# Performance work log

Measured on AMD Instinct MI355X. Metric: run time of the kernel, lower is better.

## Reference

```python
import jax, jax.numpy as jnp
import numpy as np

LMAX = 2
MUL = 8          # output_size: multiplicity of edge irreps on both TP inputs
COUT = 16        # channels_out
NB = 16          # number_of_basis
MAX_R = 5.0
NUM_PATHS = 15   # all (l1,l2,l3) triangle-valid paths with l<=2
# lexicographic path order: (0,0,0),(0,1,1),(0,2,2),(1,0,1),(1,1,0),(1,1,1),(1,1,2),
# (1,2,1),(1,2,2),(2,0,2),(2,1,1),(2,1,2),(2,2,0),(2,2,1),(2,2,2)
# x2 is zero for l2>0 (only x2[0]=Ai[dst]), so only (l,0,l) paths contribute:
PATH_IDX = {0: 0, 1: 3, 2: 9}
PATH_NORM = 1.0 / np.sqrt(MUL * MUL)  # per-path weight normalization


def silu(x):
    return jax.nn.silu(x)


def sph_harmonics(n):
    """Real spherical harmonics (component-normalized) of unit vectors n (E,3), l=0..2."""
    x, y, z = n[:, 0], n[:, 1], n[:, 2]
    Y0 = jnp.ones_like(x)[:, None]
    Y1 = jnp.sqrt(3.0) * n
    Y2 = jnp.stack([
        jnp.sqrt(15.0) * x * y,
        jnp.sqrt(15.0) * y * z,
        (jnp.sqrt(5.0) / 2.0) * (3.0 * z * z - 1.0),  # |n|=1
        jnp.sqrt(15.0) * x * z,
        (jnp.sqrt(15.0) / 2.0) * (x * x - y * y),
    ], axis=-1)
    return [Y0, Y1, Y2]


def soft_one_hot_gaussian(x, start, end, number):
    # e3nn soft_one_hot_linspace, basis='gaussian', cutoff=True
    values = jnp.linspace(start, end, number + 2)[1:-1]
    step = values[1] - values[0]
    diff = (x[:, None] - values) / step
    return jnp.exp(-diff * diff) / 1.12


def setup_inputs() -> dict:
    key = jax.random.key(0)
    ks = jax.random.split(key, 24)
    N, E, G = 50000, 800000, 64
    inp = {}
    inp["pos"] = jax.random.normal(ks[0], (N, 3), jnp.float32) * 3.0
    inp["A"] = jax.random.randint(ks[1], (N,), 0, 10)
    inp["batch"] = jnp.sort(jax.random.randint(ks[2], (N,), 0, G))
    inp["edge_src"] = jax.random.randint(ks[3], (E,), 0, N)
    inp["edge_dst"] = jax.random.randint(ks[4], (E,), 0, N)
    inp["edge_shifts"] = jnp.zeros((E, 3), jnp.float32)
    inp["cell"] = jax.random.normal(ks[5], (G, 3, 3), jnp.float32)
    # learned parameters
    inp["emb_table"] = jax.random.normal(ks[6], (10, 16), jnp.float32)
    inp["atom_w1"] = jax.random.normal(ks[7], (16, 64), jnp.float32) / 4.0
    inp["atom_b1"] = jnp.zeros((64,), jnp.float32)
    inp["atom_w2"] = jax.random.normal(ks[8], (64, MUL), jnp.float32) / 8.0
    inp["atom_b2"] = jnp.zeros((MUL,), jnp.float32)
    inp["fc_w1"] = jax.random.normal(ks[9], (NB, 64), jnp.float32) / 4.0
    inp["fc_b1"] = jnp.zeros((64,), jnp.float32)
    inp["fc_w2"] = jax.random.normal(ks[10], (64, 64), jnp.float32) / 8.0
    inp["fc_b2"] = jnp.zeros((64,), jnp.float32)
    inp["fc_w3"] = jax.random.normal(ks[11], (64, NUM_PATHS), jnp.float32) / 8.0
    inp["fc_b3"] = jnp.zeros((NUM_PATHS,), jnp.float32)
    inp["tp_w"] = jax.random.normal(ks[12], (NUM_PATHS, MUL, MUL, COUT), jnp.float32)
    return inp


def reference(pos, A, batch, edge_src, edge_dst, edge_shifts, cell,
              emb_table, atom_w1, atom_b1, atom_w2, atom_b2,
              fc_w1, fc_b1, fc_w2, fc_b2, fc_w3, fc_b3, tp_w):
    N = pos.shape[0]
    # --- edge geometry (PBC) ---
    edge_cells = cell[batch[edge_src]]                      # (E,3,3)
    shift_vecs = jnp.einsum('ei,eij->ej', edge_shifts, edge_cells)
    edge_vec = pos[edge_dst] - pos[edge_src] + shift_vecs    # (E,3)
    edge_length = jnp.sqrt(jnp.sum(edge_vec * edge_vec, axis=-1))
    n = edge_vec / jnp.maximum(edge_length, 1e-8)[:, None]
    # --- node scalars ---
    h = silu(emb_table[A] @ atom_w1 + atom_b1)
    Ai = h @ atom_w2 + atom_b2                               # (N,MUL)
    # --- spherical harmonics / per-edge irreps ---
    Y = sph_harmonics(n)                                     # list of (E,2l+1)
    Ai_src = Ai[edge_src]                                    # (E,MUL)
    x2_0 = Ai[edge_dst]                                      # (E,MUL) = only nonzero block of input 2
    # --- radial gates ---
    emb = soft_one_hot_gaussian(edge_length, 0.0, MAX_R, NB) * np.sqrt(NB)
    g = silu(emb @ fc_w1 + fc_b1)
    g = silu(g @ fc_w2 + fc_b2)
    gates = g @ fc_w3 + fc_b3                                # (E,NUM_PATHS)
    # --- tensor product: f_in[l] (x) x2[0] -> out[l]; only (l,0,l) paths survive ---
    out_parts = []
    for l in range(LMAX + 1):
        f_l = Ai_src[:, :, None] * Y[l][:, None, :]          # (E,MUL,2l+1)
        W = tp_w[PATH_IDX[l]]                                 # (MUL,MUL,COUT)
        mixed = jnp.einsum('ev,uvw->euw', x2_0, W)            # (E,MUL,COUT)
        o = jnp.einsum('eui,euw->ewi', f_l, mixed)            # (E,COUT,2l+1)
        o = o * (gates[:, PATH_IDX[l]][:, None, None] * PATH_NORM)
        out_parts.append(o.reshape(o.shape[0], COUT * (2 * l + 1)))
    edge_features = jnp.concatenate(out_parts, axis=-1)      # (E, COUT*9)
    # --- mean aggregation onto destination nodes ---
    ones = jnp.ones((edge_dst.shape[0],), edge_features.dtype)
    count = jnp.clip(jax.ops.segment_sum(ones, edge_dst, num_segments=N), 1.0)
    out = jax.ops.segment_sum(edge_features, edge_dst, num_segments=N) / count[:, None]
    return out
```

## Files before the change

### kernel.cpp

```cpp
#include <hip/hip_runtime.h>
#include <hip/hip_bf16.h>
#include <math.h>

#define MUL 8
#define NCOL 144
#define TSIZE 8192
#define TMAXLEN 8.0f
#define STG 68

__device__ __forceinline__ float silu_f(float x) { return x / (1.0f + __expf(-x)); }

__global__ void node_mlp_kernel(const int* __restrict__ A,
                                const float* __restrict__ emb_table,
                                const float* __restrict__ w1,
                                const float* __restrict__ b1,
                                const float* __restrict__ w2,
                                const float* __restrict__ b2,
                                float* __restrict__ Ai, int N) {
    __shared__ float s_w1[16 * 64];
    __shared__ float s_w2[64 * MUL];
    __shared__ float s_b1[64];
    __shared__ float s_b2[MUL];
    __shared__ float s_emb[10 * 16];
    for (int i = threadIdx.x; i < 16 * 64; i += blockDim.x) s_w1[i] = w1[i];
    for (int i = threadIdx.x; i < 64 * MUL; i += blockDim.x) s_w2[i] = w2[i];
    for (int i = threadIdx.x; i < 64; i += blockDim.x) s_b1[i] = b1[i];
    for (int i = threadIdx.x; i < MUL; i += blockDim.x) s_b2[i] = b2[i];
    for (int i = threadIdx.x; i < 160; i += blockDim.x) s_emb[i] = emb_table[i];
    __syncthreads();

    int n = blockIdx.x * blockDim.x + threadIdx.x;
    if (n >= N) return;
    int a = A[n];

    float h[64];
    #pragma unroll
    for (int j = 0; j < 64; j++) h[j] = s_b1[j];
    #pragma unroll 1
    for (int k = 0; k < 16; k++) {
        float ek = s_emb[a * 16 + k];
        #pragma unroll
        for (int j = 0; j < 64; j++) h[j] += ek * s_w1[k * 64 + j];
    }
    #pragma unroll
    for (int j = 0; j < 64; j++) h[j] = silu_f(h[j]);

    #pragma unroll 1
    for (int u = 0; u < MUL; u++) {
        float acc = s_b2[u];
        #pragma unroll
        for (int k = 0; k < 64; k++) acc += h[k] * s_w2[k * MUL + u];
        Ai[n * MUL + u] = acc;
    }
}

__global__ void __launch_bounds__(256) prologue2_kernel(
        const int* __restrict__ edst, const float* __restrict__ shifts,
        const float* __restrict__ emb_table,
        const float* __restrict__ aw1, const float* __restrict__ ab1,
        const float* __restrict__ aw2, const float* __restrict__ ab2,
        const float* __restrict__ fw1, const float* __restrict__ fb1,
        const float* __restrict__ fw2, const float* __restrict__ fb2,
        const float* __restrict__ fw3, const float* __restrict__ fb3,
        const float* __restrict__ tpw,
        int* __restrict__ count, int* __restrict__ rank, int* __restrict__ flag,
        float* __restrict__ At, float4* __restrict__ tab,
        float* __restrict__ tpwT, int E) {
    int b = blockIdx.x;
    if (b < 32) {
        int i = b * 256 + threadIdx.x;
        if (i >= TSIZE) return;
        float len = (float)i * (TMAXLEN / TSIZE);
        float r = len * (17.0f / 5.0f);
        float h[64];
        #pragma unroll
        for (int j = 0; j < 64; j++) h[j] = fb1[j];
        #pragma unroll 1
        for (int k = 0; k < 16; k++) {
            float dk = r - (float)(k + 1);
            float ek = __expf(-dk * dk) * (4.0f / 1.12f);
            #pragma unroll
            for (int j = 0; j < 64; j++) h[j] += ek * fw1[k * 64 + j];
        }
        #pragma unroll
        for (int j = 0; j < 64; j++) h[j] = silu_f(h[j]);
        float g0 = fb3[0], g1 = fb3[3], g2 = fb3[9];
        #pragma unroll 1
        for (int j = 0; j < 64; j++) {
            float a = fb2[j];
            #pragma unroll
            for (int k = 0; k < 64; k++) a += h[k] * fw2[k * 64 + j];
            a = silu_f(a);
            g0 += a * fw3[j * 15 + 0];
            g1 += a * fw3[j * 15 + 3];
            g2 += a * fw3[j * 15 + 9];
        }
        tab[i] = make_float4(g0 * 0.125f, g1 * 0.125f, g2 * 0.125f, 0.f);
    } else if (b == 32) {
        const int pl[3] = {0, 3, 9};
        for (int i = threadIdx.x; i < 3072; i += 256) {
            int l = i >> 10, r = i & 1023;
            int u = r >> 7, v = (r >> 4) & 7, w = r & 15;
            tpwT[(l << 10) + (u << 7) + (w << 3) + v] = tpw[pl[l] * 1024 + r];
        }
        int t = threadIdx.x;
        if (t < 80) {
            int ty = t >> 3, u = t & 7;
            float h[64];
            #pragma unroll
            for (int j = 0; j < 64; j++) h[j] = ab1[j];
            #pragma unroll 1
            for (int k = 0; k < 16; k++) {
                float ek = emb_table[ty * 16 + k];
                #pragma unroll
                for (int j = 0; j < 64; j++) h[j] += ek * aw1[k * 64 + j];
            }
            #pragma unroll
            for (int j = 0; j < 64; j++) h[j] = silu_f(h[j]);
            float acc = ab2[u];
            #pragma unroll
            for (int k = 0; k < 64; k++) acc += h[k] * aw2[k * MUL + u];
            At[ty * 8 + u] = acc;
        }
    } else {
        int e = (b - 33) * 256 + threadIdx.x;
        bool nz = false;
        if (e < E) {
            int d = edst[e];
            float sh0 = shifts[e * 3 + 0], sh1 = shifts[e * 3 + 1], sh2 = shifts[e * 3 + 2];
            nz = (sh0 != 0.f) || (sh1 != 0.f) || (sh2 != 0.f);
            rank[e] = atomicAdd(&count[d], 1);
        }
        if (__ballot(nz)) {
            if ((threadIdx.x & 63) == 0) atomicOr(flag, 1);
        }
    }
}

__global__ void count_kernel(const int* __restrict__ edst, int* __restrict__ count, int E) {
    int e = blockIdx.x * blockDim.x + threadIdx.x;
    if (e < E) atomicAdd(&count[edst[e]], 1);
}

__global__ void scan_kernel(const int* __restrict__ count, int* __restrict__ off, int N) {
    __shared__ int sums[1024];
    int L = N + 1;
    int chunk = (L + 1023) / 1024;
    int t = threadIdx.x;
    int lo = t * chunk;
    int hi = lo + chunk; if (hi > L) hi = L;
    int local = 0;
    for (int i = lo; i < hi; i++) local += (i < N) ? count[i] : 0;
    sums[t] = local;
    __syncthreads();
    for (int s = 1; s < 1024; s <<= 1) {
        int v = (t >= s) ? sums[t - s] : 0;
        __syncthreads();
        sums[t] += v;
        __syncthreads();
    }
    int run = (t == 0) ? 0 : sums[t - 1];
    for (int i = lo; i < hi; i++) {
        off[i] = run;
        run += (i < N) ? count[i] : 0;
    }
}

__global__ void __launch_bounds__(256) scan_part_kernel(
        const int* __restrict__ count, int* __restrict__ bsum, int N) {
    __shared__ int red[256];
    int t = threadIdx.x;
    int idx = blockIdx.x * 256 + t;
    red[t] = (idx < N) ? count[idx] : 0;
    __syncthreads();
    #pragma unroll
    for (int s = 128; s > 0; s >>= 1) {
        if (t < s) red[t] += red[t + s];
        __syncthreads();
    }
    if (t == 0) bsum[blockIdx.x] = red[0];
}

__global__ void __launch_bounds__(1024) scan_top_kernel(
        const int* __restrict__ bsum, int* __restrict__ bpre,
        int* __restrict__ off, int N, int nblk) {
    __shared__ int s[1024];
    int t = threadIdx.x;
    int v = (t < nblk) ? bsum[t] : 0;
    s[t] = v;
    __syncthreads();
    for (int d = 1; d < 1024; d <<= 1) {
        int x = (t >= d) ? s[t - d] : 0;
        __syncthreads();
        s[t] += x;
        __syncthreads();
    }
    if (t < nblk) bpre[t] = s[t] - v;
    if (t == 1023) off[N] = s[1023];
}

__global__ void __launch_bounds__(256) scan_write_kernel(
        const int* __restrict__ count, const int* __restrict__ bpre,
        int* __restrict__ off, int N) {
    __shared__ int s[256];
    int t = threadIdx.x;
    int idx = blockIdx.x * 256 + t;
    int c = (idx < N) ? count[idx] : 0;
    s[t] = c;
    __syncthreads();
    for (int d = 1; d < 256; d <<= 1) {
        int x = (t >= d) ? s[t - d] : 0;
        __syncthreads();
        s[t] += x;
        __syncthreads();
    }
    if (idx < N) off[idx] = bpre[blockIdx.x] + s[t] - c;
}

__global__ void fill_kernel(const int* __restrict__ edst, const int* __restrict__ off,
                            int* __restrict__ cursor, int* __restrict__ list, int E) {
    int e = blockIdx.x * blockDim.x + threadIdx.x;
    if (e >= E) return;
    int d = edst[e];
    int p = atomicAdd(&cursor[d], 1);
    list[off[d] + p] = e;
}

__global__ void __launch_bounds__(256) permute_kernel(
        const int* __restrict__ edst, const int* __restrict__ esrc,
        const int* __restrict__ rank, const int* __restrict__ off,
        const int* __restrict__ flagp, int* __restrict__ list, int E) {
    int e = blockIdx.x * 256 + threadIdx.x;
    if (e >= E) return;
    int d = edst[e];
    int p = off[d] + rank[e];
    list[p] = (*flagp) ? e : esrc[e];
}

__global__ void __launch_bounds__(256) conv_at_kernel(
        const float* __restrict__ pos, const int* __restrict__ batch,
        const int* __restrict__ esrc,
        const float* __restrict__ shifts, const float* __restrict__ cell,
        const int* __restrict__ A, const float* __restrict__ At,
        const float* __restrict__ tpwT, const float4* __restrict__ gtab,
        const int* __restrict__ flagp, const int* __restrict__ off,
        const int* __restrict__ list,
        float* __restrict__ out, int N) {
    __shared__ float s_stage[4][17 * STG];
    __shared__ float s_Z[4][288];
    __shared__ float s_M[4][388];
    __shared__ float s_Ad[4][32];

    const int tid = threadIdx.x, wv = tid >> 6, lane = tid & 63;
    const int k = lane >> 4, s = lane & 15;
    const int base = blockIdx.x * 16 + wv * 4;
    const int n = base + k;
    const bool nv = (n < N);

    const int FL = *flagp;

    int b0 = nv ? off[n] : 0;
    int b1 = nv ? off[n + 1] : 0;
    int deg = b1 - b0;

    if (s < 8) {
        int an = nv ? A[n] : 0;
        s_Ad[wv][k * 8 + s] = nv ? At[an * 8 + s] : 0.f;
    }

    float px = 0.f, py = 0.f, pz = 0.f;
    if (nv && deg > 0) { px = pos[n * 3 + 0]; py = pos[n * 3 + 1]; pz = pos[n * 3 + 2]; }

    int md = deg;
    md = max(md, __shfl_xor(md, 16));
    md = max(md, __shfl_xor(md, 32));
    int nrnd = (md + 15) >> 4;

    float* st = s_stage[wv];

    float z[5];
    const float4* ruP[5];
    const float4* riP[5];
    #pragma unroll
    for (int j = 0; j < 5; j++) {
        int p = s + 16 * j;
        int u = (p < 72) ? (p / 9) : 0;
        int i = (p < 72) ? (p - 9 * u) : 0;
        ruP[j] = (const float4*)(st + u * STG + k * 16);
        riP[j] = (const float4*)(st + (8 + i) * STG + k * 16);
        z[j] = 0.f;
    }

    #pragma unroll 1
    for (int rnd = 0; rnd < nrnd; rnd++) {
        int sl = (rnd << 4) + s;
        float As[8], gy[9];
        #pragma unroll
        for (int u = 0; u < 8; u++) As[u] = 0.f;
        #pragma unroll
        for (int i = 0; i < 9; i++) gy[i] = 0.f;
        if (sl < deg) {
            int v = list[b0 + sl];
            int src;
            float sv0 = 0.f, sv1 = 0.f, sv2 = 0.f;
            if (FL) {
                int e = v;
                src = esrc[e];
                float sh0 = shifts[e * 3 + 0], sh1 = shifts[e * 3 + 1], sh2 = shifts[e * 3 + 2];
                if (sh0 != 0.f || sh1 != 0.f || sh2 != 0.f) {
                    int g = batch[src];
                    const float* cg = cell + g * 9;
                    sv0 = sh0 * cg[0] + sh1 * cg[3] + sh2 * cg[6];
                    sv1 = sh0 * cg[1] + sh1 * cg[4] + sh2 * cg[7];
                    sv2 = sh0 * cg[2] + sh1 * cg[5] + sh2 * cg[8];
                }
            } else {
                src = v;
            }
            float vx = px - pos[src * 3 + 0] + sv0;
            float vy = py - pos[src * 3 + 1] + sv1;
            float vz = pz - pos[src * 3 + 2] + sv2;
            float len = sqrtf(vx * vx + vy * vy + vz * vz);
            float inv = 1.0f / fmaxf(len, 1e-8f);
            float nx = vx * inv, ny = vy * inv, nz = vz * inv;

            float tp = fminf(len * ((float)TSIZE / TMAXLEN), (float)(TSIZE - 1));
            int ti = (int)tp; if (ti > TSIZE - 2) ti = TSIZE - 2;
            float fr = tp - (float)ti;
            float4 ga = gtab[ti], gb = gtab[ti + 1];
            float g0 = ga.x + fr * (gb.x - ga.x);
            float g1 = ga.y + fr * (gb.y - ga.y);
            float g2 = ga.z + fr * (gb.z - ga.z);

            const float s3c = 1.7320508075688772f;
            const float s15 = 3.872983346207417f;
            const float s5h = 1.118033988749895f;
            gy[0] = g0;
            gy[1] = g1 * (s3c * nx); gy[2] = g1 * (s3c * ny); gy[3] = g1 * (s3c * nz);
            gy[4] = g2 * (s15 * nx * ny); gy[5] = g2 * (s15 * ny * nz);
            gy[6] = g2 * (s5h * (3.f * nz * nz - 1.f));
            gy[7] = g2 * (s15 * nx * nz); gy[8] = g2 * (0.5f * s15 * (nx * nx - ny * ny));

            int a = A[src];
            const float4* Ap = (const float4*)(At + a * 8);
            float4 A0 = Ap[0], A1 = Ap[1];
            As[0] = A0.x; As[1] = A0.y; As[2] = A0.z; As[3] = A0.w;
            As[4] = A1.x; As[5] = A1.y; As[6] = A1.z; As[7] = A1.w;
        }
        #pragma unroll
        for (int u = 0; u < 8; u++) st[u * STG + lane] = As[u];
        #pragma unroll
        for (int i = 0; i < 9; i++) st[(8 + i) * STG + lane] = gy[i];
        __builtin_amdgcn_wave_barrier();
        #pragma unroll
        for (int j = 0; j < 5; j++) {
            if (j < 4 || s < 8) {
                #pragma unroll
                for (int c = 0; c < 4; c++) {
                    float4 a = ruP[j][c], b = riP[j][c];
                    z[j] += a.x * b.x + a.y * b.y + a.z * b.z + a.w * b.w;
                }
            }
        }
        __builtin_amdgcn_wave_barrier();
    }

    #pragma unroll
    for (int j = 0; j < 5; j++)
        if (j < 4 || s < 8) s_Z[wv][k * 72 + s + 16 * j] = z[j];
    __builtin_amdgcn_wave_barrier();

    const float4* twp[6];
    int moff[6];
    #pragma unroll
    for (int t = 0; t < 6; t++) {
        int m = lane + (t << 6);
        int l = m >> 7, r = m & 127, u = r >> 4, w = r & 15;
        twp[t] = (const float4*)(tpwT + (l << 10) + (u << 7) + (w << 3));
        moff[t] = (l << 7) + (w << 3) + u;
    }
    int moffo[3], zoff[3];
    bool ov[3];
    #pragma unroll
    for (int t = 0; t < 3; t++) {
        int c = lane + (t << 6);
        ov[t] = (c < NCOL);
        int cc = ov[t] ? c : 0;
        int l, w, ii;
        if (cc < 16)      { l = 0; w = cc;            ii = 0; }
        else if (cc < 64) { l = 1; w = (cc - 16) / 3; ii = 1 + (cc - 16) % 3; }
        else              { l = 2; w = (cc - 64) / 5; ii = 4 + (cc - 64) % 5; }
        moffo[t] = (l << 7) + (w << 3);
        zoff[t] = ii;
    }

    float* M = s_M[wv];
    float* Zb = s_Z[wv];
    #pragma unroll 1
    for (int k2 = 0; k2 < 4; k2++) {
        int nk = base + k2;
        float Adk[8];
        #pragma unroll
        for (int v = 0; v < 8; v++) Adk[v] = s_Ad[wv][k2 * 8 + v];
        #pragma unroll
        for (int t = 0; t < 6; t++) {
            float4 wa = twp[t][0], wb = twp[t][1];
            M[moff[t]] = Adk[0] * wa.x + Adk[1] * wa.y + Adk[2] * wa.z + Adk[3] * wa.w
                       + Adk[4] * wb.x + Adk[5] * wb.y + Adk[6] * wb.z + Adk[7] * wb.w;
        }
        int degk = __shfl(deg, k2 * 16);
        __builtin_amdgcn_wave_barrier();
        if (nk < N) {
            float dinv = 1.0f / fmaxf((float)degk, 1.0f);
            const float* Zk = Zb + k2 * 72;
            #pragma unroll
            for (int t = 0; t < 3; t++) {
                if (ov[t]) {
                    const float4* mm = (const float4*)(M + moffo[t]);
                    float4 m0 = mm[0], m1 = mm[1];
                    int ii = zoff[t];
                    float val = m0.x * Zk[0 + ii]  + m0.y * Zk[9 + ii]
                              + m0.z * Zk[18 + ii] + m0.w * Zk[27 + ii]
                              + m1.x * Zk[36 + ii] + m1.y * Zk[45 + ii]
                              + m1.z * Zk[54 + ii] + m1.w * Zk[63 + ii];
                    out[(size_t)nk * NCOL + lane + (t << 6)] = val * dinv;
                }
            }
        }
        __builtin_amdgcn_wave_barrier();
    }
}

__global__ void __launch_bounds__(256) prologue_kernel(
        const int* __restrict__ A, const float* __restrict__ emb_table,
        const float* __restrict__ aw1, const float* __restrict__ ab1,
        const float* __restrict__ aw2, const float* __restrict__ ab2,
        const float* __restrict__ fw1, const float* __restrict__ fb1,
        const float* __restrict__ fw2, const float* __restrict__ fb2,
        const float* __restrict__ fw3, const float* __restrict__ fb3,
        const float* __restrict__ tpw,
        float* __restrict__ Ai, float4* __restrict__ tab,
        float* __restrict__ tpwT, int N) {
    __shared__ float s_w1[16 * 64];
    __shared__ float s_w2[64 * MUL];
    __shared__ float s_b1[64];
    __shared__ float s_b2[MUL];
    __shared__ float s_emb[10 * 16];

    int b = blockIdx.x;
    if (b < 32) {
        int i = b * 256 + threadIdx.x;
        if (i >= TSIZE) return;
        float len = (float)i * (TMAXLEN / TSIZE);
        float r = len * (17.0f / 5.0f);
        float h[64];
        #pragma unroll
        for (int j = 0; j < 64; j++) h[j] = fb1[j];
        #pragma unroll 1
        for (int k = 0; k < 16; k++) {
            float dk = r - (float)(k + 1);
            float ek = __expf(-dk * dk) * (4.0f / 1.12f);
            #pragma unroll
            for (int j = 0; j < 64; j++) h[j] += ek * fw1[k * 64 + j];
        }
        #pragma unroll
        for (int j = 0; j < 64; j++) h[j] = silu_f(h[j]);
        float g0 = fb3[0], g1 = fb3[3], g2 = fb3[9];
        #pragma unroll 1
        for (int j = 0; j < 64; j++) {
            float a = fb2[j];
            #pragma unroll
            for (int k = 0; k < 64; k++) a += h[k] * fw2[k * 64 + j];
            a = silu_f(a);
            g0 += a * fw3[j * 15 + 0];
            g1 += a * fw3[j * 15 + 3];
            g2 += a * fw3[j * 15 + 9];
        }
        tab[i] = make_float4(g0 * 0.125f, g1 * 0.125f, g2 * 0.125f, 0.f);
    } else if (b == 32) {
        const int pl[3] = {0, 3, 9};
        for (int i = threadIdx.x; i < 3072; i += 256) {
            int l = i >> 10, r = i & 1023;
            int u = r >> 7, v = (r >> 4) & 7, w = r & 15;
            tpwT[(l << 10) + (u << 7) + (w << 3) + v] = tpw[pl[l] * 1024 + r];
        }
    } else {
        for (int i = threadIdx.x; i < 16 * 64; i += 256) s_w1[i] = aw1[i];
        for (int i = threadIdx.x; i < 64 * MUL; i += 256) s_w2[i] = aw2[i];
        for (int i = threadIdx.x; i < 64; i += 256) s_b1[i] = ab1[i];
        for (int i = threadIdx.x; i < MUL; i += 256) s_b2[i] = ab2[i];
        for (int i = threadIdx.x; i < 160; i += 256) s_emb[i] = emb_table[i];
        __syncthreads();

        int n = (b - 33) * 256 + threadIdx.x;
        if (n >= N) return;
        int a = A[n];

        float h[64];
        #pragma unroll
        for (int j = 0; j < 64; j++) h[j] = s_b1[j];
        #pragma unroll 1
        for (int k = 0; k < 16; k++) {
            float ek = s_emb[a * 16 + k];
            #pragma unroll
            for (int j = 0; j < 64; j++) h[j] += ek * s_w1[k * 64 + j];
        }
        #pragma unroll
        for (int j = 0; j < 64; j++) h[j] = silu_f(h[j]);

        #pragma unroll 1
        for (int u = 0; u < MUL; u++) {
            float acc = s_b2[u];
            #pragma unroll
            for (int k = 0; k < 64; k++) acc += h[k] * s_w2[k * MUL + u];
            Ai[n * MUL + u] = acc;
        }
    }
}

__global__ void __launch_bounds__(256) conv_node4_kernel(
        const float* __restrict__ pos, const int* __restrict__ batch,
        const int* __restrict__ esrc,
        const float* __restrict__ shifts, const float* __restrict__ cell,
        const float* __restrict__ tpwT, const float4* __restrict__ gtab,
        const float* __restrict__ Ai, const int* __restrict__ off,
        const int* __restrict__ list,
        float* __restrict__ out, int N) {
    __shared__ float s_stage[4][17 * STG];
    __shared__ float s_Z[4][288];
    __shared__ float s_M[4][388];
    __shared__ float s_Ad[4][32];

    const int tid = threadIdx.x, wv = tid >> 6, lane = tid & 63;
    const int k = lane >> 4, s = lane & 15;
    const int base = blockIdx.x * 16 + wv * 4;
    const int n = base + k;
    const bool nv = (n < N);

    int b0 = nv ? off[n] : 0;
    int b1 = nv ? off[n + 1] : 0;
    int deg = b1 - b0;

    if (s < 8) s_Ad[wv][k * 8 + s] = nv ? Ai[(size_t)n * MUL + s] : 0.f;

    float px = 0.f, py = 0.f, pz = 0.f;
    if (nv && deg > 0) { px = pos[n * 3 + 0]; py = pos[n * 3 + 1]; pz = pos[n * 3 + 2]; }

    int md = deg;
    md = max(md, __shfl_xor(md, 16));
    md = max(md, __shfl_xor(md, 32));
    int nrnd = (md + 15) >> 4;

    float* st = s_stage[wv];

    float z[5];
    const float4* ruP[5];
    const float4* riP[5];
    #pragma unroll
    for (int j = 0; j < 5; j++) {
        int p = s + 16 * j;
        int u = (p < 72) ? (p / 9) : 0;
        int i = (p < 72) ? (p - 9 * u) : 0;
        ruP[j] = (const float4*)(st + u * STG + k * 16);
        riP[j] = (const float4*)(st + (8 + i) * STG + k * 16);
        z[j] = 0.f;
    }

    #pragma unroll 1
    for (int rnd = 0; rnd < nrnd; rnd++) {
        int sl = (rnd << 4) + s;
        float As[8], gy[9];
        #pragma unroll
        for (int u = 0; u < 8; u++) As[u] = 0.f;
        #pragma unroll
        for (int i = 0; i < 9; i++) gy[i] = 0.f;
        if (sl < deg) {
            int e = list[b0 + sl];
            float sh0 = shifts[e * 3 + 0], sh1 = shifts[e * 3 + 1], sh2 = shifts[e * 3 + 2];
            int src = esrc[e];
            float sv0 = 0.f, sv1 = 0.f, sv2 = 0.f;
            if (sh0 != 0.f || sh1 != 0.f || sh2 != 0.f) {
                int g = batch[src];
                const float* cg = cell + g * 9;
                sv0 = sh0 * cg[0] + sh1 * cg[3] + sh2 * cg[6];
                sv1 = sh0 * cg[1] + sh1 * cg[4] + sh2 * cg[7];
                sv2 = sh0 * cg[2] + sh1 * cg[5] + sh2 * cg[8];
            }
            float vx = px - pos[src * 3 + 0] + sv0;
            float vy = py - pos[src * 3 + 1] + sv1;
            float vz = pz - pos[src * 3 + 2] + sv2;
            float len = sqrtf(vx * vx + vy * vy + vz * vz);
            float inv = 1.0f / fmaxf(len, 1e-8f);
            float nx = vx * inv, ny = vy * inv, nz = vz * inv;

            float tp = fminf(len * ((float)TSIZE / TMAXLEN), (float)(TSIZE - 1));
            int ti = (int)tp; if (ti > TSIZE - 2) ti = TSIZE - 2;
            float fr = tp - (float)ti;
            float4 ga = gtab[ti], gb = gtab[ti + 1];
            float g0 = ga.x + fr * (gb.x - ga.x);
            float g1 = ga.y + fr * (gb.y - ga.y);
            float g2 = ga.z + fr * (gb.z - ga.z);

            const float s3c = 1.7320508075688772f;
            const float s15 = 3.872983346207417f;
            const float s5h = 1.118033988749895f;
            gy[0] = g0;
            gy[1] = g1 * (s3c * nx); gy[2] = g1 * (s3c * ny); gy[3] = g1 * (s3c * nz);
            gy[4] = g2 * (s15 * nx * ny); gy[5] = g2 * (s15 * ny * nz);
            gy[6] = g2 * (s5h * (3.f * nz * nz - 1.f));
            gy[7] = g2 * (s15 * nx * nz); gy[8] = g2 * (0.5f * s15 * (nx * nx - ny * ny));

            const float4* Ap = (const float4*)(Ai + (size_t)src * MUL);
            float4 A0 = Ap[0], A1 = Ap[1];
            As[0] = A0.x; As[1] = A0.y; As[2] = A0.z; As[3] = A0.w;
            As[4] = A1.x; As[5] = A1.y; As[6] = A1.z; As[7] = A1.w;
        }
        #pragma unroll
        for (int u = 0; u < 8; u++) st[u * STG + lane] = As[u];
        #pragma unroll
        for (int i = 0; i < 9; i++) st[(8 + i) * STG + lane] = gy[i];
        __builtin_amdgcn_wave_barrier();
        #pragma unroll
        for (int j = 0; j < 5; j++) {
            if (j < 4 || s < 8) {
                #pragma unroll
                for (int c = 0; c < 4; c++) {
                    float4 a = ruP[j][c], b = riP[j][c];
                    z[j] += a.x * b.x + a.y * b.y + a.z * b.z + a.w * b.w;
                }
            }
        }
        __builtin_amdgcn_wave_barrier();
    }

    #pragma unroll
    for (int j = 0; j < 5; j++)
        if (j < 4 || s < 8) s_Z[wv][k * 72 + s + 16 * j] = z[j];
    __builtin_amdgcn_wave_barrier();

    const float4* twp[6];
    int moff[6];
    #pragma unroll
    for (int t = 0; t < 6; t++) {
        int m = lane + (t << 6);
        int l = m >> 7, r = m & 127, u = r >> 4, w = r & 15;
        twp[t] = (const float4*)(tpwT + (l << 10) + (u << 7) + (w << 3));
        moff[t] = (l << 7) + (w << 3) + u;
    }
    int moffo[3], zoff[3];
    bool ov[3];
    #pragma unroll
    for (int t = 0; t < 3; t++) {
        int c = lane + (t << 6);
        ov[t] = (c < NCOL);
        int cc = ov[t] ? c : 0;
        int l, w, ii;
        if (cc < 16)      { l = 0; w = cc;            ii = 0; }
        else if (cc < 64) { l = 1; w = (cc - 16) / 3; ii = 1 + (cc - 16) % 3; }
        else              { l = 2; w = (cc - 64) / 5; ii = 4 + (cc - 64) % 5; }
        moffo[t] = (l << 7) + (w << 3);
        zoff[t] = ii;
    }

    float* M = s_M[wv];
    float* Zb = s_Z[wv];
    #pragma unroll 1
    for (int k2 = 0; k2 < 4; k2++) {
        int nk = base + k2;
        float Adk[8];
        #pragma unroll
        for (int v = 0; v < 8; v++) Adk[v] = s_Ad[wv][k2 * 8 + v];
        #pragma unroll
        for (int t = 0; t < 6; t++) {
            float4 wa = twp[t][0], wb = twp[t][1];
            M[moff[t]] = Adk[0] * wa.x + Adk[1] * wa.y + Adk[2] * wa.z + Adk[3] * wa.w
                       + Adk[4] * wb.x + Adk[5] * wb.y + Adk[6] * wb.z + Adk[7] * wb.w;
        }
        int degk = __shfl(deg, k2 * 16);
        __builtin_amdgcn_wave_barrier();
        if (nk < N) {
            float dinv = 1.0f / fmaxf((float)degk, 1.0f);
            const float* Zk = Zb + k2 * 72;
            #pragma unroll
            for (int t = 0; t < 3; t++) {
                if (ov[t]) {
                    const float4* mm = (const float4*)(M + moffo[t]);
                    float4 m0 = mm[0], m1 = mm[1];
                    int ii = zoff[t];
                    float val = m0.x * Zk[0 + ii]  + m0.y * Zk[9 + ii]
                              + m0.z * Zk[18 + ii] + m0.w * Zk[27 + ii]
                              + m1.x * Zk[36 + ii] + m1.y * Zk[45 + ii]
                              + m1.z * Zk[54 + ii] + m1.w * Zk[63 + ii];
                    out[(size_t)nk * NCOL + lane + (t << 6)] = val * dinv;
                }
            }
        }
        __builtin_amdgcn_wave_barrier();
    }
}

__global__ void __launch_bounds__(256) edge_atomic_kernel(
        const float* __restrict__ pos, const int* __restrict__ batch,
        const int* __restrict__ esrc, const int* __restrict__ edst,
        const float* __restrict__ shifts, const float* __restrict__ cell,
        const float* __restrict__ fw1, const float* __restrict__ fb1,
        const float* __restrict__ fw2, const float* __restrict__ fb2,
        const float* __restrict__ fw3, const float* __restrict__ fb3,
        const float* __restrict__ tpw,
        const float* __restrict__ Ai,
        float* __restrict__ out, float* __restrict__ deg, int E) {
    __shared__ float s_w1[16 * 64];
    __shared__ float s_w2[64 * 64];
    __shared__ float s_w3[64 * 3];
    __shared__ float s_b1[64];
    __shared__ float s_b2[64];
    __shared__ float s_b3[3];
    __shared__ float s_tpw[3 * 1024];
    for (int i = threadIdx.x; i < 1024; i += blockDim.x) s_w1[i] = fw1[i];
    for (int i = threadIdx.x; i < 4096; i += blockDim.x) s_w2[i] = fw2[i];
    for (int i = threadIdx.x; i < 64; i += blockDim.x) { s_b1[i] = fb1[i]; s_b2[i] = fb2[i]; }
    for (int i = threadIdx.x; i < 192; i += blockDim.x) {
        int j = i / 3, c = i - 3 * j;
        int cc = (c == 0) ? 0 : ((c == 1) ? 3 : 9);
        s_w3[i] = fw3[j * 15 + cc];
    }
    if (threadIdx.x < 3) {
        int cc = (threadIdx.x == 0) ? 0 : ((threadIdx.x == 1) ? 3 : 9);
        s_b3[threadIdx.x] = fb3[cc];
    }
    for (int i = threadIdx.x; i < 3 * 1024; i += blockDim.x) {
        int l = i >> 10, r = i & 1023;
        int p = (l == 0) ? 0 : ((l == 1) ? 3 : 9);
        s_tpw[i] = tpw[p * 1024 + r];
    }
    __syncthreads();
    int e = blockIdx.x * blockDim.x + threadIdx.x;
    if (e >= E) return;
    int s = esrc[e], d = edst[e];
    int g = batch[s];
    float sh0 = shifts[e * 3 + 0], sh1 = shifts[e * 3 + 1], sh2 = shifts[e * 3 + 2];
    const float* cg = cell + g * 9;
    float sv0 = sh0 * cg[0] + sh1 * cg[3] + sh2 * cg[6];
    float sv1 = sh0 * cg[1] + sh1 * cg[4] + sh2 * cg[7];
    float sv2 = sh0 * cg[2] + sh1 * cg[5] + sh2 * cg[8];
    float vx = pos[d * 3 + 0] - pos[s * 3 + 0] + sv0;
    float vy = pos[d * 3 + 1] - pos[s * 3 + 1] + sv1;
    float vz = pos[d * 3 + 2] - pos[s * 3 + 2] + sv2;
    float len = sqrtf(vx * vx + vy * vy + vz * vz);
    float inv = 1.0f / fmaxf(len, 1e-8f);
    float nx = vx * inv, ny = vy * inv, nz = vz * inv;
    float r = len * (17.0f / 5.0f);
    float h[64];
    #pragma unroll
    for (int j = 0; j < 64; j++) h[j] = s_b1[j];
    #pragma unroll 1
    for (int k = 0; k < 16; k++) {
        float dk = r - (float)(k + 1);
        float ek = __expf(-dk * dk) * (4.0f / 1.12f);
        #pragma unroll
        for (int j = 0; j < 64; j++) h[j] += ek * s_w1[k * 64 + j];
    }
    #pragma unroll
    for (int j = 0; j < 64; j++) h[j] = silu_f(h[j]);
    float g0 = s_b3[0], g1 = s_b3[1], g2 = s_b3[2];
    #pragma unroll 2
    for (int j = 0; j < 64; j++) {
        float a = s_b2[j];
        #pragma unroll
        for (int k = 0; k < 64; k++) a += h[k] * s_w2[k * 64 + j];
        a = silu_f(a);
        g0 += a * s_w3[j * 3 + 0];
        g1 += a * s_w3[j * 3 + 1];
        g2 += a * s_w3[j * 3 + 2];
    }
    g0 *= 0.125f; g1 *= 0.125f; g2 *= 0.125f;
    float t0[16], t1[16], t2[16];
    #pragma unroll
    for (int w = 0; w < 16; w++) { t0[w] = 0.f; t1[w] = 0.f; t2[w] = 0.f; }
    int s8 = s * MUL, d8 = d * MUL;
    float Ad[8];
    #pragma unroll
    for (int v = 0; v < 8; v++) Ad[v] = Ai[d8 + v];
    #pragma unroll 1
    for (int u = 0; u < 8; u++) {
        float asu = Ai[s8 + u];
        int offp = u * 128;
        #pragma unroll
        for (int v = 0; v < 8; v++) {
            float p = asu * Ad[v];
            int o2 = offp + v * 16;
            #pragma unroll
            for (int w = 0; w < 16; w++) {
                t0[w] += p * s_tpw[o2 + w];
                t1[w] += p * s_tpw[1024 + o2 + w];
                t2[w] += p * s_tpw[2048 + o2 + w];
            }
        }
    }
    #pragma unroll
    for (int w = 0; w < 16; w++) { t0[w] *= g0; t1[w] *= g1; t2[w] *= g2; }
    const float s3 = 1.7320508075688772f;
    const float s15 = 3.872983346207417f;
    const float s5h = 1.118033988749895f;
    float y1_[3] = { s3 * nx, s3 * ny, s3 * nz };
    float y2_[5] = { s15 * nx * ny, s15 * ny * nz, s5h * (3.f * nz * nz - 1.f),
                     s15 * nx * nz, 0.5f * s15 * (nx * nx - ny * ny) };
    float* o = out + (size_t)d * NCOL;
    #pragma unroll
    for (int w = 0; w < 16; w++) atomicAdd(o + w, t0[w]);
    #pragma unroll
    for (int w = 0; w < 16; w++)
        #pragma unroll
        for (int i = 0; i < 3; i++) atomicAdd(o + 16 + w * 3 + i, t1[w] * y1_[i]);
    #pragma unroll
    for (int w = 0; w < 16; w++)
        #pragma unroll
        for (int i = 0; i < 5; i++) atomicAdd(o + 64 + w * 5 + i, t2[w] * y2_[i]);
    atomicAdd(deg + d, 1.0f);
}

__global__ void finalize_kernel(float* __restrict__ out, const float* __restrict__ deg, int total) {
    int idx = blockIdx.x * blockDim.x + threadIdx.x;
    if (idx >= total) return;
    int n = idx / NCOL;
    out[idx] = out[idx] / fmaxf(deg[n], 1.0f);
}

extern "C" void kernel_launch(void* const* d_in, const int* in_sizes, int n_in,
                              void* d_out, int out_size, void* d_ws, size_t ws_size,
                              hipStream_t stream) {
    const float* pos    = (const float*)d_in[0];
    const int*   A      = (const int*)d_in[1];
    const int*   batch  = (const int*)d_in[2];
    const int*   esrc   = (const int*)d_in[3];
    const int*   edst   = (const int*)d_in[4];
    const float* shifts = (const float*)d_in[5];
    const float* cellp  = (const float*)d_in[6];
    const float* embt   = (const float*)d_in[7];
    const float* aw1    = (const float*)d_in[8];
    const float* ab1    = (const float*)d_in[9];
    const float* aw2    = (const float*)d_in[10];
    const float* ab2    = (const float*)d_in[11];
    const float* fw1    = (const float*)d_in[12];
    const float* fb1    = (const float*)d_in[13];
    const float* fw2    = (const float*)d_in[14];
    const float* fb2    = (const float*)d_in[15];
    const float* fw3    = (const float*)d_in[16];
    const float* fb3    = (const float*)d_in[17];
    const float* tpw    = (const float*)d_in[18];

    int N = in_sizes[1];
    int E = in_sizes[3];
    float* out = (float*)d_out;

    int nblk = (N + 255) / 256;
    int eblk = (E + 255) / 256;

    size_t need_new = ((size_t)N + 1 + (size_t)(N + 1) + (size_t)E * 2) * 4
                    + (size_t)TSIZE * 16 + 3072 * 4 + 320 + 8192 + 768;
    size_t need_mid = (size_t)N * 32 + (size_t)N * 8 + (size_t)(N + 1) * 4
                    + (size_t)E * 4 + (size_t)TSIZE * 16 + 3072 * 4 + 8192 + 1024;

    if (ws_size >= need_new && nblk <= 1024) {
        int*    count = (int*)d_ws;
        int*    flag  = count + N;
        int*    off   = flag + 1;
        int*    rank  = off + (N + 1);
        int*    list  = rank + E;
        float4* gtab  = (float4*)(((uintptr_t)(list + E) + 255) & ~(uintptr_t)255);
        float*  tpwT  = (float*)(gtab + TSIZE);
        float*  At    = tpwT + 3072;
        int*    bsum  = (int*)(At + 80);
        int*    bpre  = bsum + 1024;

        hipMemsetAsync(count, 0, ((size_t)N + 1) * sizeof(int), stream);

        prologue2_kernel<<<33 + eblk, 256, 0, stream>>>(
            edst, shifts, embt, aw1, ab1, aw2, ab2,
            fw1, fb1, fw2, fb2, fw3, fb3, tpw,
            count, rank, flag, At, gtab, tpwT, E);

        scan_part_kernel<<<nblk, 256, 0, stream>>>(count, bsum, N);
        scan_top_kernel<<<1, 1024, 0, stream>>>(bsum, bpre, off, N, nblk);
        scan_write_kernel<<<nblk, 256, 0, stream>>>(count, bpre, off, N);

        permute_kernel<<<eblk, 256, 0, stream>>>(edst, esrc, rank, off, flag, list, E);

        conv_at_kernel<<<(N + 15) / 16, 256, 0, stream>>>(
            pos, batch, esrc, shifts, cellp, A, At, tpwT, gtab, flag, off, list, out, N);
    } else if (ws_size >= need_mid) {
        float*  Ai     = (float*)d_ws;
        int*    count  = (int*)(Ai + (size_t)N * MUL);
        int*    cursor = count + N;
        int*    off    = cursor + N;
        int*    list   = off + (N + 1);
        float4* gtab   = (float4*)(((uintptr_t)(list + E) + 255) & ~(uintptr_t)255);
        float*  tpwT   = (float*)(gtab + TSIZE);
        int*    bsum   = (int*)(tpwT + 3072);
        int*    bpre   = bsum + 1024;

        hipMemsetAsync(count, 0, (size_t)N * 2 * sizeof(int), stream);

        prologue_kernel<<<33 + nblk, 256, 0, stream>>>(
            A, embt, aw1, ab1, aw2, ab2, fw1, fb1, fw2, fb2, fw3, fb3,
            tpw, Ai, gtab, tpwT, N);
        count_kernel<<<eblk, 256, 0, stream>>>(edst, count, E);

        if (nblk <= 1024) {
            scan_part_kernel<<<nblk, 256, 0, stream>>>(count, bsum, N);
            scan_top_kernel<<<1, 1024, 0, stream>>>(bsum, bpre, off, N, nblk);
            scan_write_kernel<<<nblk, 256, 0, stream>>>(count, bpre, off, N);
        } else {
            scan_kernel<<<1, 1024, 0, stream>>>(count, off, N);
        }

        fill_kernel<<<eblk, 256, 0, stream>>>(edst, off, cursor, list, E);

        conv_node4_kernel<<<(N + 15) / 16, 256, 0, stream>>>(
            pos, batch, esrc, shifts, cellp, tpwT, gtab, Ai, off, list, out, N);
    } else {
        float* Ai  = (float*)d_ws;
        float* deg = Ai + (size_t)N * MUL;
        hipMemsetAsync(out, 0, (size_t)out_size * sizeof(float), stream);
        hipMemsetAsync(deg, 0, (size_t)N * sizeof(float), stream);
        node_mlp_kernel<<<(N + 255) / 256, 256, 0, stream>>>(A, embt, aw1, ab1, aw2, ab2, Ai, N);
        edge_atomic_kernel<<<eblk, 256, 0, stream>>>(
            pos, batch, esrc, edst, shifts, cellp,
            fw1, fb1, fw2, fb2, fw3, fb3, tpw, Ai, out, deg, E);
        int total = N * NCOL;
        finalize_kernel<<<(total + 255) / 256, 256, 0, stream>>>(out, deg, total);
    }
}
```

Measured before the change: 218.1 us.

## Parallelize gate-table MLP across wavefront lanes instead of per-thread serial loops

```diff
diff --git a/kernel.cpp b/kernel.cpp
--- a/kernel.cpp
+++ b/kernel.cpp
@@ -7,6 +7,7 @@
 #define TSIZE 8192
 #define TMAXLEN 8.0f
 #define STG 68
+#define GBLK 512
 
 __device__ __forceinline__ float silu_f(float x) { return x / (1.0f + __expf(-x)); }
 
@@ -54,7 +55,7 @@
     }
 }
 
-__global__ void __launch_bounds__(256) prologue2_kernel(
+__global__ void __launch_bounds__(256) front_kernel(
         const int* __restrict__ edst, const float* __restrict__ shifts,
         const float* __restrict__ emb_table,
         const float* __restrict__ aw1, const float* __restrict__ ab1,
@@ -66,64 +67,68 @@
         int* __restrict__ count, int* __restrict__ rank, int* __restrict__ flag,
         float* __restrict__ At, float4* __restrict__ tab,
         float* __restrict__ tpwT, int E) {
-    int b = blockIdx.x;
-    if (b < 32) {
-        int i = b * 256 + threadIdx.x;
-        if (i >= TSIZE) return;
-        float len = (float)i * (TMAXLEN / TSIZE);
-        float r = len * (17.0f / 5.0f);
-        float h[64];
-        #pragma unroll
-        for (int j = 0; j < 64; j++) h[j] = fb1[j];
+    const int b = blockIdx.x;
+    const int lane = threadIdx.x & 63, wv = threadIdx.x >> 6;
+
+    if (b < GBLK) {
+        int gw = b * 4 + wv;
         #pragma unroll 1
-        for (int k = 0; k < 16; k++) {
-            float dk = r - (float)(k + 1);
-            float ek = __expf(-dk * dk) * (4.0f / 1.12f);
-            #pragma unroll
-            for (int j = 0; j < 64; j++) h[j] += ek * fw1[k * 64 + j];
-        }
-        #pragma unroll
-        for (int j = 0; j < 64; j++) h[j] = silu_f(h[j]);
-        float g0 = fb3[0], g1 = fb3[3], g2 = fb3[9];
-        #pragma unroll 1
-        for (int j = 0; j < 64; j++) {
-            float a = fb2[j];
-            #pragma unroll
-            for (int k = 0; k < 64; k++) a += h[k] * fw2[k * 64 + j];
+        for (int e = gw; e < TSIZE; e += GBLK * 4) {
+            float len = (float)e * (TMAXLEN / TSIZE);
+            float r = len * (17.0f / 5.0f);
+            float h = fb1[lane];
+            #pragma unroll
+            for (int k = 0; k < 16; k++) {
+                float dk = r - (float)(k + 1);
+                float ek = __expf(-dk * dk) * (4.0f / 1.12f);
+                h += ek * fw1[k * 64 + lane];
+            }
+            h = silu_f(h);
+            float a = fb2[lane];
+            #pragma unroll
+            for (int k = 0; k < 64; k++) a += __shfl(h, k) * fw2[k * 64 + lane];
             a = silu_f(a);
-            g0 += a * fw3[j * 15 + 0];
-            g1 += a * fw3[j * 15 + 3];
-            g2 += a * fw3[j * 15 + 9];
-        }
-        tab[i] = make_float4(g0 * 0.125f, g1 * 0.125f, g2 * 0.125f, 0.f);
-    } else if (b == 32) {
+            float g0 = a * fw3[lane * 15 + 0];
+            float g1 = a * fw3[lane * 15 + 3];
+            float g2 = a * fw3[lane * 15 + 9];
+            #pragma unroll
+            for (int off = 32; off > 0; off >>= 1) {
+                g0 += __shfl_xor(g0, off);
+                g1 += __shfl_xor(g1, off);
+                g2 += __shfl_xor(g2, off);
+            }
+            if (lane == 0)
+                tab[e] = make_float4((fb3[0] + g0) * 0.125f,
+                                     (fb3[3] + g1) * 0.125f,
+                                     (fb3[9] + g2) * 0.125f, 0.f);
+        }
+    } else if (b == GBLK) {
         const int pl[3] = {0, 3, 9};
         for (int i = threadIdx.x; i < 3072; i += 256) {
             int l = i >> 10, r = i & 1023;
             int u = r >> 7, v = (r >> 4) & 7, w = r & 15;
             tpwT[(l << 10) + (u << 7) + (w << 3) + v] = tpw[pl[l] * 1024 + r];
         }
-        int t = threadIdx.x;
-        if (t < 80) {
-            int ty = t >> 3, u = t & 7;
-            float h[64];
-            #pragma unroll
-            for (int j = 0; j < 64; j++) h[j] = ab1[j];
-            #pragma unroll 1
-            for (int k = 0; k < 16; k++) {
-                float ek = emb_table[ty * 16 + k];
+        #pragma unroll 1
+        for (int ty = wv; ty < 10; ty += 4) {
+            float h = ab1[lane];
+            #pragma unroll
+            for (int k = 0; k < 16; k++) h += emb_table[ty * 16 + k] * aw1[k * 64 + lane];
+            h = silu_f(h);
+            float p[8];
+            #pragma unroll
+            for (int u = 0; u < 8; u++) p[u] = h * aw2[lane * MUL + u];
+            #pragma unroll
+            for (int off = 32; off > 0; off >>= 1)
                 #pragma unroll
-                for (int j = 0; j < 64; j++) h[j] += ek * aw1[k * 64 + j];
+                for (int u = 0; u < 8; u++) p[u] += __shfl_xor(p[u], off);
+            if (lane == 0) {
+                #pragma unroll
+                for (int u = 0; u < 8; u++) At[ty * MUL + u] = ab2[u] + p[u];
             }
-            #pragma unroll
-            for (int j = 0; j < 64; j++) h[j] = silu_f(h[j]);
-            float acc = ab2[u];
-            #pragma unroll
-            for (int k = 0; k < 64; k++) acc += h[k] * aw2[k * MUL + u];
-            At[ty * 8 + u] = acc;
         }
     } else {
-        int e = (b - 33) * 256 + threadIdx.x;
+        int e = (b - GBLK - 1) * 256 + threadIdx.x;
         bool nz = false;
         if (e < E) {
             int d = edst[e];
@@ -132,7 +137,7 @@
             rank[e] = atomicAdd(&count[d], 1);
         }
         if (__ballot(nz)) {
-            if ((threadIdx.x & 63) == 0) atomicOr(flag, 1);
+            if (lane == 0) atomicOr(flag, 1);
         }
     }
 }
@@ -875,7 +880,7 @@
 
         hipMemsetAsync(count, 0, ((size_t)N + 1) * sizeof(int), stream);
 
-        prologue2_kernel<<<33 + eblk, 256, 0, stream>>>(
+        front_kernel<<<GBLK + 1 + eblk, 256, 0, stream>>>(
             edst, shifts, embt, aw1, ab1, aw2, ab2,
             fw1, fb1, fw2, fb2, fw3, fb3, tpw,
             count, rank, flag, At, gtab, tpwT, E);
```

Result: faster. 199.9 us (-8.3%).
